# Kernel optimization log

Measured on AMD Instinct MI355X. Metric: run time of the kernel, lower is better.

The kernel has to match this reference:

```python
import jax, jax.numpy as jnp
import numpy as np

B = 1024
N = 100  # graph_size
D = 128


def setup_inputs() -> dict:
    key = jax.random.key(0)
    k1, k2 = jax.random.split(key)
    x = jax.random.normal(k1, (B * N, D), dtype=jnp.float32)
    edge_index = jax.random.randint(k2, (2, B * N * (N - 1)), 0, N, dtype=jnp.int64)
    return {"x": x, "edge_index": edge_index, "graph_size": N}


def reference(x, edge_index, graph_size):
    # x: [B*N, D] -> [B, N, D]; edge_index is split but never used in the math.
    b = x.shape[0] // graph_size
    xb = x.reshape(b, graph_size, -1)
    # per-graph dot-product logits: [B, N, N]
    logits = jnp.einsum('bnd,bmd->bnm', xb, xb)
    # segment softmax with index j = column index of the flattened [N*N] logits:
    # normalizes over rows i for each column j -> softmax along axis=1.
    return jax.nn.softmax(logits, axis=1)
```

## Files before the change

### kernel.cpp

```cpp
#include <hip/hip_runtime.h>

#define NG 100
#define DD 128
#define NPAD 112
#define LSTRIDE 136

typedef __attribute__((ext_vector_type(8))) short bf16x8;
typedef __attribute__((ext_vector_type(4))) float floatx4;

__device__ __forceinline__ unsigned int f2bf(float f) {
    unsigned int u = __float_as_uint(f);
    return (u + 0x7FFFu + ((u >> 16) & 1u)) >> 16;
}

__global__ __launch_bounds__(256, 4)
void dotdec_mfma(const float* __restrict__ x, float* __restrict__ out) {
    __shared__ unsigned short xs[NPAD * LSTRIDE];
    const int t    = threadIdx.x;
    const int lane = t & 63;
    const int wave = t >> 6;
    const int quad = lane >> 4;
    const int lr   = lane & 15;
    const size_t b = blockIdx.x;
    const float* xb = x   + b * (size_t)(NG * DD);
    float*       ob = out + b * (size_t)(NG * NG);

    for (int i = t; i < 12 * 64; i += 256) {
        int r = 100 + (i >> 6), cp = i & 63;
        *(unsigned int*)&xs[r * LSTRIDE + cp * 2] = 0u;
    }
#pragma unroll
    for (int k = 0; k < 13; ++k) {
        int flat = t + 256 * k;
        if (flat < NG * 32) {
            int n = flat >> 5, g = flat & 31;
            float4 v = ((const float4*)xb)[flat];
            unsigned int p0 = f2bf(v.x) | (f2bf(v.y) << 16);
            unsigned int p1 = f2bf(v.z) | (f2bf(v.w) << 16);
            *(uint2*)&xs[n * LSTRIDE + g * 4] = make_uint2(p0, p1);
        }
    }
    __syncthreads();

    const int c0 = wave;
    const int c1 = (wave < 3) ? wave + 4 : wave;
    floatx4 acc[2][7];
#pragma unroll
    for (int ci = 0; ci < 2; ++ci)
#pragma unroll
        for (int t2 = 0; t2 < 7; ++t2) acc[ci][t2] = (floatx4){0.f, 0.f, 0.f, 0.f};

#pragma unroll
    for (int k = 0; k < 4; ++k) {
        const int koff = k * 32 + quad * 8;
        bf16x8 b0 = *(const bf16x8*)&xs[(c0 * 16 + lr) * LSTRIDE + koff];
        bf16x8 b1 = *(const bf16x8*)&xs[(c1 * 16 + lr) * LSTRIDE + koff];
#pragma unroll
        for (int t2 = 0; t2 < 7; ++t2) {
            bf16x8 a = *(const bf16x8*)&xs[(t2 * 16 + lr) * LSTRIDE + koff];
            acc[0][t2] = __builtin_amdgcn_mfma_f32_16x16x32_bf16(a, b0, acc[0][t2], 0, 0, 0);
            acc[1][t2] = __builtin_amdgcn_mfma_f32_16x16x32_bf16(a, b1, acc[1][t2], 0, 0, 0);
        }
    }

    float mx0 = -3.402823466e38f, mx1 = -3.402823466e38f;
#pragma unroll
    for (int t2 = 0; t2 < 6; ++t2)
#pragma unroll
        for (int i = 0; i < 4; ++i) {
            mx0 = fmaxf(mx0, acc[0][t2][i]);
            mx1 = fmaxf(mx1, acc[1][t2][i]);
        }
    if (quad == 0)
#pragma unroll
        for (int i = 0; i < 4; ++i) {
            mx0 = fmaxf(mx0, acc[0][6][i]);
            mx1 = fmaxf(mx1, acc[1][6][i]);
        }
    mx0 = fmaxf(mx0, __shfl_xor(mx0, 16, 64));
    mx0 = fmaxf(mx0, __shfl_xor(mx0, 32, 64));
    mx1 = fmaxf(mx1, __shfl_xor(mx1, 16, 64));
    mx1 = fmaxf(mx1, __shfl_xor(mx1, 32, 64));

    float s0 = 0.f, s1 = 0.f;
#pragma unroll
    for (int t2 = 0; t2 < 6; ++t2)
#pragma unroll
        for (int i = 0; i < 4; ++i) {
            float e0 = __expf(acc[0][t2][i] - mx0); acc[0][t2][i] = e0; s0 += e0;
            float e1 = __expf(acc[1][t2][i] - mx1); acc[1][t2][i] = e1; s1 += e1;
        }
    if (quad == 0)
#pragma unroll
        for (int i = 0; i < 4; ++i) {
            float e0 = __expf(acc[0][6][i] - mx0); acc[0][6][i] = e0; s0 += e0;
            float e1 = __expf(acc[1][6][i] - mx1); acc[1][6][i] = e1; s1 += e1;
        }
    s0 += __shfl_xor(s0, 16, 64); s0 += __shfl_xor(s0, 32, 64);
    s1 += __shfl_xor(s1, 16, 64); s1 += __shfl_xor(s1, 32, 64);
    const float r0 = 1.f / s0;
    const float r1 = 1.f / s1;

    const int m0 = c0 * 16 + lr;
    const int m1 = c1 * 16 + lr;
    const bool dual = (c1 != c0) && (m1 < NG);
#pragma unroll
    for (int t2 = 0; t2 < 6; ++t2)
#pragma unroll
        for (int i = 0; i < 4; ++i) {
            int n = t2 * 16 + quad * 4 + i;
            ob[n * NG + m0] = acc[0][t2][i] * r0;
            if (dual) ob[n * NG + m1] = acc[1][t2][i] * r1;
        }
    if (quad == 0)
#pragma unroll
        for (int i = 0; i < 4; ++i) {
            int n = 96 + i;
            ob[n * NG + m0] = acc[0][6][i] * r0;
            if (dual) ob[n * NG + m1] = acc[1][6][i] * r1;
        }
}

extern "C" void kernel_launch(void* const* d_in, const int* in_sizes, int n_in,
                              void* d_out, int out_size, void* d_ws, size_t ws_size,
                              hipStream_t stream) {
    const float* x = (const float*)d_in[0];
    float* out = (float*)d_out;
    const int B = in_sizes[0] / (NG * DD);
    hipLaunchKernelGGL(dotdec_mfma, dim3(B), dim3(256), 0, stream, x, out);
}
```

Baseline: 157.0 us.

## Stage softmax output through LDS for coalesced float4 stores; truncate bf16

```diff
diff --git a/kernel.cpp b/kernel.cpp
--- a/kernel.cpp
+++ b/kernel.cpp
@@ -8,14 +8,12 @@
 typedef __attribute__((ext_vector_type(8))) short bf16x8;
 typedef __attribute__((ext_vector_type(4))) float floatx4;
 
-__device__ __forceinline__ unsigned int f2bf(float f) {
-    unsigned int u = __float_as_uint(f);
-    return (u + 0x7FFFu + ((u >> 16) & 1u)) >> 16;
-}
-
 __global__ __launch_bounds__(256, 4)
 void dotdec_mfma(const float* __restrict__ x, float* __restrict__ out) {
-    __shared__ unsigned short xs[NPAD * LSTRIDE];
+    __shared__ __align__(16) char smraw[NG * NG * 4];
+    unsigned short* xs = (unsigned short*)smraw;
+    float*          fo = (float*)smraw;
+
     const int t    = threadIdx.x;
     const int lane = t & 63;
     const int wave = t >> 6;
@@ -25,19 +23,22 @@
     const float* xb = x   + b * (size_t)(NG * DD);
     float*       ob = out + b * (size_t)(NG * NG);
 
-    for (int i = t; i < 12 * 64; i += 256) {
-        int r = 100 + (i >> 6), cp = i & 63;
-        *(unsigned int*)&xs[r * LSTRIDE + cp * 2] = 0u;
+    if (t < 192) {
+        int r = 100 + (t >> 4), c = t & 15;
+        *(uint4*)&xs[r * LSTRIDE + c * 8] = make_uint4(0u, 0u, 0u, 0u);
     }
 #pragma unroll
-    for (int k = 0; k < 13; ++k) {
-        int flat = t + 256 * k;
-        if (flat < NG * 32) {
-            int n = flat >> 5, g = flat & 31;
-            float4 v = ((const float4*)xb)[flat];
-            unsigned int p0 = f2bf(v.x) | (f2bf(v.y) << 16);
-            unsigned int p1 = f2bf(v.z) | (f2bf(v.w) << 16);
-            *(uint2*)&xs[n * LSTRIDE + g * 4] = make_uint2(p0, p1);
+    for (int k = 0; k < 7; ++k) {
+        int p = t + 256 * k;
+        if (p < NG * 16) {
+            int n = p >> 4, gp = p & 15;
+            float4 v0 = ((const float4*)xb)[n * 32 + gp * 2];
+            float4 v1 = ((const float4*)xb)[n * 32 + gp * 2 + 1];
+            unsigned int u0 = (__float_as_uint(v0.x) >> 16) | (__float_as_uint(v0.y) & 0xffff0000u);
+            unsigned int u1 = (__float_as_uint(v0.z) >> 16) | (__float_as_uint(v0.w) & 0xffff0000u);
+            unsigned int u2 = (__float_as_uint(v1.x) >> 16) | (__float_as_uint(v1.y) & 0xffff0000u);
+            unsigned int u3 = (__float_as_uint(v1.z) >> 16) | (__float_as_uint(v1.w) & 0xffff0000u);
+            *(uint4*)&xs[n * LSTRIDE + gp * 8] = make_uint4(u0, u1, u2, u3);
         }
     }
     __syncthreads();
@@ -98,9 +99,10 @@
         }
     s0 += __shfl_xor(s0, 16, 64); s0 += __shfl_xor(s0, 32, 64);
     s1 += __shfl_xor(s1, 16, 64); s1 += __shfl_xor(s1, 32, 64);
-    const float r0 = 1.f / s0;
-    const float r1 = 1.f / s1;
+    const float r0 = __builtin_amdgcn_rcpf(s0);
+    const float r1 = __builtin_amdgcn_rcpf(s1);
 
+    __syncthreads();
     const int m0 = c0 * 16 + lr;
     const int m1 = c1 * 16 + lr;
     const bool dual = (c1 != c0) && (m1 < NG);
@@ -109,16 +111,26 @@
 #pragma unroll
         for (int i = 0; i < 4; ++i) {
             int n = t2 * 16 + quad * 4 + i;
-            ob[n * NG + m0] = acc[0][t2][i] * r0;
-            if (dual) ob[n * NG + m1] = acc[1][t2][i] * r1;
+            fo[n * NG + m0] = acc[0][t2][i] * r0;
+            if (dual) fo[n * NG + m1] = acc[1][t2][i] * r1;
         }
     if (quad == 0)
 #pragma unroll
         for (int i = 0; i < 4; ++i) {
             int n = 96 + i;
-            ob[n * NG + m0] = acc[0][6][i] * r0;
-            if (dual) ob[n * NG + m1] = acc[1][6][i] * r1;
+            fo[n * NG + m0] = acc[0][6][i] * r0;
+            if (dual) fo[n * NG + m1] = acc[1][6][i] * r1;
         }
+    __syncthreads();
+
+#pragma unroll
+    for (int k = 0; k < 10; ++k) {
+        int f = t + 256 * k;
+        if (f < (NG * NG) / 4) {
+            float4 v = *(const float4*)&fo[f * 4];
+            ((float4*)ob)[f] = v;
+        }
+    }
 }
 
 extern "C" void kernel_launch(void* const* d_in, const int* in_sizes, int n_in,
```

Result: no change. 155.7 us (-0.8%).
